# Kernel tuning notes

Hardware: AMD Instinct MI355X
Metric: run time of the kernel (lower is better)

The kernel has to match this reference:

```python
import jax, jax.numpy as jnp
import numpy as np

B, S, D, H = 1, 4096, 512, 8
HD = D // H  # head_dims = 64


def setup_inputs() -> dict:
    key = jax.random.key(0)
    ks = jax.random.split(key, 12)
    scale = 0.02
    query = jax.random.normal(ks[0], (B, S, D), dtype=jnp.float32)
    key_t = jax.random.normal(ks[1], (B, S, D), dtype=jnp.float32)
    value = jax.random.normal(ks[2], (B, S, D), dtype=jnp.float32)
    mask = jax.random.randint(ks[3], (B, 1, S, S), 0, 2, dtype=jnp.int32)
    # per-head projection params (torch Linear: y = x @ W.T + b)
    Wq = jax.random.normal(ks[4], (HD, HD), dtype=jnp.float32) * scale
    bq = jax.random.normal(ks[5], (HD,), dtype=jnp.float32) * scale
    Wk = jax.random.normal(ks[6], (HD, HD), dtype=jnp.float32) * scale
    bk = jax.random.normal(ks[7], (HD,), dtype=jnp.float32) * scale
    Wv = jax.random.normal(ks[8], (HD, HD), dtype=jnp.float32) * scale
    bv = jax.random.normal(ks[9], (HD,), dtype=jnp.float32) * scale
    Wfc = jax.random.normal(ks[10], (D, D), dtype=jnp.float32) * scale
    bfc = jax.random.normal(ks[11], (D,), dtype=jnp.float32) * scale
    return {"query": query, "key": key_t, "value": value, "mask": mask,
            "Wq": Wq, "bq": bq, "Wk": Wk, "bk": bk, "Wv": Wv, "bv": bv,
            "Wfc": Wfc, "bfc": bfc}


def reference(query, key, value, mask, Wq, bq, Wk, bk, Wv, bv, Wfc, bfc):
    Batch, q_len, _ = query.shape
    k_len = key.shape[1]
    # reshape to [b, s, h, d] then apply per-head linear projections
    q = query.reshape(Batch, q_len, H, HD) @ Wq.T + bq
    k = key.reshape(Batch, k_len, H, HD) @ Wk.T + bk
    v = value.reshape(Batch, k_len, H, HD) @ Wv.T + bv
    # raw scores [b, h, q, k]; mask applied BEFORE scaling (as in original)
    score = jnp.einsum('bqhd,bkhd->bhqk', q, k)
    score = jnp.where(mask == 0, jnp.float32(-1e20), score)
    attn = jax.nn.softmax(score / jnp.sqrt(jnp.float32(HD)), axis=-1)
    out = jnp.einsum('bhqv,bvhd->bqhd', attn, v).reshape(Batch, q_len, D)
    return out @ Wfc.T + bfc
```

## Files before the change

### kernel.cpp

```cpp
#include <hip/hip_runtime.h>
#include <hip/hip_bf16.h>

#define S_LEN 4096
#define DMODEL 512
#define NHEAD 8
#define HDIM 64

typedef __bf16 bf16x8 __attribute__((ext_vector_type(8)));
typedef __bf16 bf16x4 __attribute__((ext_vector_type(4)));
typedef float f32x4 __attribute__((ext_vector_type(4)));

#define S2EXP 0.18033688011112042f

__device__ __forceinline__ void gload_lds16(const void* g, void* l) {
    __builtin_amdgcn_global_load_lds((const __attribute__((address_space(1))) void*)g,
                                     (__attribute__((address_space(3))) void*)l, 16, 0, 0);
}

__global__ __launch_bounds__(256) void proj_all_kernel(const float* __restrict__ xq,
                                                       const float* __restrict__ xk,
                                                       const float* __restrict__ xv,
                                                       const float* __restrict__ Wq,
                                                       const float* __restrict__ bq,
                                                       const float* __restrict__ Wk,
                                                       const float* __restrict__ bk,
                                                       const float* __restrict__ Wv,
                                                       const float* __restrict__ bv,
                                                       __bf16* __restrict__ yq,
                                                       __bf16* __restrict__ yk,
                                                       __bf16* __restrict__ vt) {
    __shared__ float T[64][65];
    int bid = blockIdx.x;
    int t = threadIdx.x, wave = t >> 6, lane = t & 63, lg = lane >> 4, lc = lane & 15;
    if (bid < 512) {
        int r0 = bid * 64 + wave * 16;
        const float* xrq = xq + (size_t)(r0 + lc) * 64 + lg * 8;
        const float* xrk = xk + (size_t)(r0 + lc) * 64 + lg * 8;
        bf16x8 aq[2], ak[2];
#pragma unroll
        for (int c = 0; c < 2; ++c) {
            f32x4 u0 = *(const f32x4*)(xrq + c * 32);
            f32x4 u1 = *(const f32x4*)(xrq + c * 32 + 4);
            f32x4 v0 = *(const f32x4*)(xrk + c * 32);
            f32x4 v1 = *(const f32x4*)(xrk + c * 32 + 4);
            bf16x8 a, b;
#pragma unroll
            for (int j = 0; j < 4; ++j) {
                a[j] = (__bf16)u0[j]; a[4 + j] = (__bf16)u1[j];
                b[j] = (__bf16)v0[j]; b[4 + j] = (__bf16)v1[j];
            }
            aq[c] = a; ak[c] = b;
        }
#pragma unroll
        for (int nt = 0; nt < 4; ++nt) {
            const float* wq = Wq + (size_t)(nt * 16 + lc) * 64 + lg * 8;
            const float* wk = Wk + (size_t)(nt * 16 + lc) * 64 + lg * 8;
            f32x4 cq = {0, 0, 0, 0}, ck = {0, 0, 0, 0};
#pragma unroll
            for (int c = 0; c < 2; ++c) {
                f32x4 u0 = *(const f32x4*)(wq + c * 32);
                f32x4 u1 = *(const f32x4*)(wq + c * 32 + 4);
                f32x4 v0 = *(const f32x4*)(wk + c * 32);
                f32x4 v1 = *(const f32x4*)(wk + c * 32 + 4);
                bf16x8 bw, bw2;
#pragma unroll
                for (int j = 0; j < 4; ++j) {
                    bw[j] = (__bf16)u0[j]; bw[4 + j] = (__bf16)u1[j];
                    bw2[j] = (__bf16)v0[j]; bw2[4 + j] = (__bf16)v1[j];
                }
                cq = __builtin_amdgcn_mfma_f32_16x16x32_bf16(aq[c], bw, cq, 0, 0, 0);
                ck = __builtin_amdgcn_mfma_f32_16x16x32_bf16(ak[c], bw2, ck, 0, 0, 0);
            }
            float bqv = bq[nt * 16 + lc], bkv = bk[nt * 16 + lc];
#pragma unroll
            for (int r = 0; r < 4; ++r) {
                yq[(size_t)(r0 + lg * 4 + r) * 64 + nt * 16 + lc] = (__bf16)((cq[r] + bqv) * S2EXP);
                yk[(size_t)(r0 + lg * 4 + r) * 64 + nt * 16 + lc] = (__bf16)(ck[r] + bkv);
            }
        }
    } else {
        int vb = bid - 512;
        int h = vb & 7, s0 = (vb >> 3) * 64;
        const float* xr = xv + ((size_t)(s0 + wave * 16 + lc) * 8 + h) * 64 + lg * 8;
        bf16x8 av[2];
#pragma unroll
        for (int c = 0; c < 2; ++c) {
            f32x4 u0 = *(const f32x4*)(xr + c * 32);
            f32x4 u1 = *(const f32x4*)(xr + c * 32 + 4);
            bf16x8 a;
#pragma unroll
            for (int j = 0; j < 4; ++j) { a[j] = (__bf16)u0[j]; a[4 + j] = (__bf16)u1[j]; }
            av[c] = a;
        }
#pragma unroll
        for (int nt = 0; nt < 4; ++nt) {
            const float* wv = Wv + (size_t)(nt * 16 + lc) * 64 + lg * 8;
            f32x4 cv = {0, 0, 0, 0};
#pragma unroll
            for (int c = 0; c < 2; ++c) {
                f32x4 u0 = *(const f32x4*)(wv + c * 32);
                f32x4 u1 = *(const f32x4*)(wv + c * 32 + 4);
                bf16x8 bw;
#pragma unroll
                for (int j = 0; j < 4; ++j) { bw[j] = (__bf16)u0[j]; bw[4 + j] = (__bf16)u1[j]; }
                cv = __builtin_amdgcn_mfma_f32_16x16x32_bf16(av[c], bw, cv, 0, 0, 0);
            }
            float bvv = bv[nt * 16 + lc];
#pragma unroll
            for (int r = 0; r < 4; ++r) T[wave * 16 + lg * 4 + r][nt * 16 + lc] = cv[r] + bvv;
        }
        __syncthreads();
        int d = t >> 2, qr = t & 3;
        bf16x8 w0, w1;
#pragma unroll
        for (int i = 0; i < 8; ++i) {
            w0[i] = (__bf16)T[qr * 16 + i][d];
            w1[i] = (__bf16)T[qr * 16 + 8 + i][d];
        }
        __bf16* dst = vt + ((size_t)h * 64 + d) * 4096 + s0 + qr * 16;
        *(bf16x8*)(dst) = w0;
        *(bf16x8*)(dst + 8) = w1;
    }
}

__global__ __launch_bounds__(256) void prep_kernel(const int* __restrict__ mask,
                                                   unsigned int* __restrict__ pack,
                                                   const float* __restrict__ Wfc,
                                                   __bf16* __restrict__ wfc_bf) {
    int bid = blockIdx.x;
    int t = threadIdx.x;
    if (bid < 2048) {
        int lane = t & 63;
        int wid = bid * 4 + (t >> 6);
#pragma unroll 4
        for (int it = 0; it < 32; ++it) {
            int gw = wid * 32 + it;
            int qi = gw >> 6, seg = gw & 63;
            unsigned long long bits = __ballot(mask[(size_t)qi * 4096 + seg * 64 + lane] != 0);
            if (lane == 0)
                *(unsigned long long*)(&pack[(size_t)qi * 128 + seg * 2]) = bits;
        }
    } else {
        int b = bid - 2048;
        const f32x4* s4 = (const f32x4*)Wfc;
#pragma unroll
        for (int i = 0; i < 8; ++i) {
            int idx = (b * 8 + i) * 256 + t;
            f32x4 v = s4[idx];
            bf16x4 o;
#pragma unroll
            for (int j = 0; j < 4; ++j) o[j] = (__bf16)v[j];
            *(bf16x4*)(wfc_bf + (size_t)idx * 4) = o;
        }
    }
}

__global__ __launch_bounds__(256, 8) void attn_kernel(const __bf16* __restrict__ qb,
                                                      const __bf16* __restrict__ kb,
                                                      const __bf16* __restrict__ vt,
                                                      const unsigned int* __restrict__ mp,
                                                      int split_steps,
                                                      float* __restrict__ opart,
                                                      float* __restrict__ stats,
                                                      __bf16* __restrict__ ao) {
    int bid = blockIdx.x;
    int h = bid & 7, qt = (bid >> 3) & 63, sp = bid >> 9;
    int kv0 = sp * split_steps * 32;
    int nsteps = min(split_steps, 128 - sp * split_steps);
    int t = threadIdx.x, wave = t >> 6, lane = t & 63, lg = lane >> 4, lc = lane & 15;
    int q0 = qt * 64 + wave * 16;

    __shared__ __bf16 Kt[2][32 * 64];
    __shared__ __bf16 Vt[2][64 * 32];
    __shared__ __bf16 P[4][16 * 32];

    int srK = lane >> 3;
    int cgK = (lane & 7) ^ srK;
    int srV = lane >> 2;
    int cgV = ((lane & 3) - ((lane >> 3) & 3)) & 3;

    const __bf16* qrow = qb + ((size_t)(q0 + lc) * 8 + h) * 64 + lg * 8;
    bf16x8 qf0 = *(const bf16x8*)(qrow);
    bf16x8 qf1 = *(const bf16x8*)(qrow + 32);

    bf16x8 onesf;
#pragma unroll
    for (int j = 0; j < 8; ++j) onesf[j] = (__bf16)1.0f;

    f32x4 o0 = {0,0,0,0}, o1 = {0,0,0,0}, o2 = {0,0,0,0}, o3 = {0,0,0,0};
    f32x4 l_acc = {0,0,0,0};

    const unsigned int* mrow = mp + (size_t)(q0 + lc) * 128;
    const __bf16* vbase = vt + (size_t)h * 64 * 4096;

    gload_lds16(kb + (size_t)(kv0 + wave * 8 + srK) * 512 + h * 64 + cgK * 8, &Kt[0][wave * 512]);
    gload_lds16(vbase + (size_t)(wave * 16 + srV) * 4096 + kv0 + cgV * 8,     &Vt[0][wave * 512]);
    __syncthreads();

    int rotP = (lc >> 1) & 3;
    int lg4 = lg * 4;
    for (int step = 0; step < nsteps; ++step) {
        int cur = step & 1;
        int kb_i = kv0 + step * 32;
        if (step < nsteps - 1) {
            int nxt = kb_i + 32;
            gload_lds16(kb + (size_t)(nxt + wave * 8 + srK) * 512 + h * 64 + cgK * 8, &Kt[cur ^ 1][wave * 512]);
            gload_lds16(vbase + (size_t)(wave * 16 + srV) * 4096 + nxt + cgV * 8,     &Vt[cur ^ 1][wave * 512]);
        }
        const char* Kb = (const char*)&Kt[cur][0];
        f32x4 sc[2];
#pragma unroll
        for (int kc = 0; kc < 2; ++kc) {
            int row = kc * 16 + lc;
            int sw = (row & 7) << 4;
            bf16x8 kf0 = *(const bf16x8*)(Kb + ((row * 128 + lg * 16) ^ sw));
            bf16x8 kf1 = *(const bf16x8*)(Kb + ((row * 128 + 64 + lg * 16) ^ sw));
            f32x4 z = {0,0,0,0};
            z = __builtin_amdgcn_mfma_f32_16x16x32_bf16(kf0, qf0, z, 0, 0, 0);
            z = __builtin_amdgcn_mfma_f32_16x16x32_bf16(kf1, qf1, z, 0, 0, 0);
            sc[kc] = z;
        }
        unsigned int mws = mrow[kb_i >> 5] >> lg4;
        char* pbase = (char*)&P[wave][0];
#pragma unroll
        for (int kc = 0; kc < 2; ++kc) {
            bf16x4 pk;
#pragma unroll
            for (int r = 0; r < 4; ++r) {
                float p = __builtin_amdgcn_exp2f(sc[kc][r]);
                int sel = __builtin_amdgcn_sbfe((int)mws, kc * 16 + r, 1);
                pk[r] = (__bf16)__int_as_float(__float_as_int(p) & sel);
            }
            int phys = ((kc * 2 + (lg >> 1)) + rotP) & 3;
            int byte = lc * 64 + phys * 16 + (lg & 1) * 8;
            *(bf16x4*)(pbase + byte) = pk;
        }
        const char* Vb = (const char*)&Vt[cur][0];
        bf16x8 pf = *(const bf16x8*)(pbase + (lc * 64 + (((lg + rotP) & 3) * 16)));
        l_acc = __builtin_amdgcn_mfma_f32_16x16x32_bf16(pf, onesf, l_acc, 0, 0, 0);
#pragma unroll
        for (int dt = 0; dt < 4; ++dt) {
            int row = dt * 16 + lc;
            bf16x8 vf = *(const bf16x8*)(Vb + (row * 64 + (((lg + rotP) & 3) * 16)));
            if (dt == 0) o0 = __builtin_amdgcn_mfma_f32_16x16x32_bf16(pf, vf, o0, 0, 0, 0);
            if (dt == 1) o1 = __builtin_amdgcn_mfma_f32_16x16x32_bf16(pf, vf, o1, 0, 0, 0);
            if (dt == 2) o2 = __builtin_amdgcn_mfma_f32_16x16x32_bf16(pf, vf, o2, 0, 0, 0);
            if (dt == 3) o3 = __builtin_amdgcn_mfma_f32_16x16x32_bf16(pf, vf, o3, 0, 0, 0);
        }
        __syncthreads();
    }
    if (opart) {
        if (lc == 0) {
#pragma unroll
            for (int r = 0; r < 4; ++r)
                stats[(size_t)sp * 32768 + (size_t)(q0 + lg * 4 + r) * 8 + h] = l_acc[r];
        }
#pragma unroll
        for (int r = 0; r < 4; ++r) {
            size_t rh = (size_t)sp * 32768 + (size_t)(q0 + lg * 4 + r) * 8 + h;
            float* dst = opart + rh * 64;
            dst[0 * 16 + lc] = o0[r];
            dst[1 * 16 + lc] = o1[r];
            dst[2 * 16 + lc] = o2[r];
            dst[3 * 16 + lc] = o3[r];
        }
    } else {
#pragma unroll
        for (int r = 0; r < 4; ++r) {
            float inv = 1.0f / l_acc[r];
            int row = q0 + lg * 4 + r;
            __bf16* dst = ao + (size_t)row * 512 + h * 64;
            dst[0 * 16 + lc] = (__bf16)(o0[r] * inv);
            dst[1 * 16 + lc] = (__bf16)(o1[r] * inv);
            dst[2 * 16 + lc] = (__bf16)(o2[r] * inv);
            dst[3 * 16 + lc] = (__bf16)(o3[r] * inv);
        }
    }
}

__global__ __launch_bounds__(256) void combine_kernel(const float* __restrict__ opart,
                                                      const float* __restrict__ stats,
                                                      __bf16* __restrict__ ao, int nsplit) {
    int t = threadIdx.x, lane = t & 63, w = t >> 6;
    int rh = blockIdx.x * 4 + w;
    float L = 0.f, acc = 0.f;
#pragma unroll 4
    for (int sp = 0; sp < nsplit; ++sp) {
        L += stats[(size_t)sp * 32768 + rh];
        acc += opart[((size_t)sp * 32768 + rh) * 64 + lane];
    }
    int row = rh >> 3, h = rh & 7;
    ao[(size_t)row * 512 + h * 64 + lane] = (__bf16)(acc / L);
}

__global__ __launch_bounds__(256) void fc_kernel(const __bf16* __restrict__ ao,
                                                 const __bf16* __restrict__ Wb,
                                                 const float* __restrict__ bfc,
                                                 float* __restrict__ out) {
    int bid = blockIdx.x;
    int stile = bid >> 3, nt = bid & 7;
    int t = threadIdx.x, wave = t >> 6, lane = t & 63, lg = lane >> 4, lc = lane & 15;
    int s0 = stile * 64 + wave * 16;
    int n0 = nt * 64;
    f32x4 c0 = {0,0,0,0}, c1 = {0,0,0,0}, c2 = {0,0,0,0}, c3 = {0,0,0,0};
    for (int k0 = 0; k0 < 512; k0 += 32) {
        bf16x8 af = *(const bf16x8*)(ao + (size_t)(s0 + lc) * 512 + k0 + lg * 8);
        const __bf16* wb = Wb + k0 + lg * 8;
        c0 = __builtin_amdgcn_mfma_f32_16x16x32_bf16(af, *(const bf16x8*)(wb + (size_t)(n0 + 0 * 16 + lc) * 512), c0, 0, 0, 0);
        c1 = __builtin_amdgcn_mfma_f32_16x16x32_bf16(af, *(const bf16x8*)(wb + (size_t)(n0 + 1 * 16 + lc) * 512), c1, 0, 0, 0);
        c2 = __builtin_amdgcn_mfma_f32_16x16x32_bf16(af, *(const bf16x8*)(wb + (size_t)(n0 + 2 * 16 + lc) * 512), c2, 0, 0, 0);
        c3 = __builtin_amdgcn_mfma_f32_16x16x32_bf16(af, *(const bf16x8*)(wb + (size_t)(n0 + 3 * 16 + lc) * 512), c3, 0, 0, 0);
    }
#pragma unroll
    for (int r = 0; r < 4; ++r) {
        int row = s0 + lg * 4 + r;
        float* dst = out + (size_t)row * 512 + n0;
        dst[0 * 16 + lc] = c0[r] + bfc[n0 + 0 * 16 + lc];
        dst[1 * 16 + lc] = c1[r] + bfc[n0 + 1 * 16 + lc];
        dst[2 * 16 + lc] = c2[r] + bfc[n0 + 2 * 16 + lc];
        dst[3 * 16 + lc] = c3[r] + bfc[n0 + 3 * 16 + lc];
    }
}

extern "C" void kernel_launch(void* const* d_in, const int* in_sizes, int n_in,
                              void* d_out, int out_size, void* d_ws, size_t ws_size,
                              hipStream_t stream) {
    const float* query = (const float*)d_in[0];
    const float* key   = (const float*)d_in[1];
    const float* value = (const float*)d_in[2];
    const int*   mask  = (const int*)d_in[3];
    const float* Wq  = (const float*)d_in[4];
    const float* bq  = (const float*)d_in[5];
    const float* Wk  = (const float*)d_in[6];
    const float* bk  = (const float*)d_in[7];
    const float* Wv  = (const float*)d_in[8];
    const float* bv  = (const float*)d_in[9];
    const float* Wfc = (const float*)d_in[10];
    const float* bfc = (const float*)d_in[11];

    char* ws = (char*)d_ws;
    const size_t MB = 1024 * 1024;
    __bf16* q_bf   = (__bf16*)(ws + 0 * MB);
    __bf16* k_bf   = (__bf16*)(ws + 4 * MB);
    __bf16* vt     = (__bf16*)(ws + 8 * MB);
    __bf16* ao     = (__bf16*)(ws + 12 * MB);
    __bf16* wfc_bf = (__bf16*)(ws + 16 * MB);
    unsigned int* mpack = (unsigned int*)(ws + 17 * MB);
    const size_t base = 19 * MB;
    int nsplit = 1, split_steps = 128;
    if (ws_size >= base + 4 * (8 * MB) + 4 * 131072)      { nsplit = 4; split_steps = 32; }
    else if (ws_size >= base + 2 * (8 * MB) + 2 * 131072) { nsplit = 2; split_steps = 64; }
    float* opart = (float*)(ws + base);
    float* stats = (float*)(ws + base + (size_t)nsplit * 8 * MB);

    proj_all_kernel<<<1024, 256, 0, stream>>>(query, key, value, Wq, bq, Wk, bk, Wv, bv,
                                              q_bf, k_bf, vt);
    prep_kernel<<<2080, 256, 0, stream>>>(mask, mpack, Wfc, wfc_bf);
    if (nsplit > 1) {
        attn_kernel<<<512 * nsplit, 256, 0, stream>>>(q_bf, k_bf, vt, mpack,
                                                      split_steps, opart, stats, ao);
        combine_kernel<<<8192, 256, 0, stream>>>(opart, stats, ao, nsplit);
    } else {
        attn_kernel<<<512, 256, 0, stream>>>(q_bf, k_bf, vt, mpack,
                                             split_steps, nullptr, nullptr, ao);
    }
    fc_kernel<<<512, 256, 0, stream>>>(ao, wfc_bf, bfc, (float*)d_out);
}
```

Measured before the change: 135.1 us.

## Deepen attention KV pipeline to four LDS stages and stage mask via LDS

Replaces the double-buffered K/V staging in the attention kernel with a four-buffer ring that prefetches two steps ahead, using explicit vmcnt waits and a single barrier per step. The loop is unrolled by four. The packed mask words are also loaded into LDS asynchronously instead of read per lane from global memory. Separately, the KV split drops from 4 to 2 and occupancy hint goes from 8 to 4 blocks, which lowers parallelism and combine traffic but increases LDS use per block and the length of each block's serial loop.

Measured after the change: 123.6 us. 8.5% less time.

```diff
diff --git a/kernel.cpp b/kernel.cpp
--- a/kernel.cpp
+++ b/kernel.cpp
@@ -15,6 +15,10 @@
 __device__ __forceinline__ void gload_lds16(const void* g, void* l) {
     __builtin_amdgcn_global_load_lds((const __attribute__((address_space(1))) void*)g,
                                      (__attribute__((address_space(3))) void*)l, 16, 0, 0);
+}
+__device__ __forceinline__ void gload_lds4(const void* g, void* l) {
+    __builtin_amdgcn_global_load_lds((const __attribute__((address_space(1))) void*)g,
+                                     (__attribute__((address_space(3))) void*)l, 4, 0, 0);
 }
 
 __global__ __launch_bounds__(256) void proj_all_kernel(const float* __restrict__ xq,
@@ -155,7 +159,7 @@
     }
 }
 
-__global__ __launch_bounds__(256, 8) void attn_kernel(const __bf16* __restrict__ qb,
+__global__ __launch_bounds__(256, 4) void attn_kernel(const __bf16* __restrict__ qb,
                                                       const __bf16* __restrict__ kb,
                                                       const __bf16* __restrict__ vt,
                                                       const unsigned int* __restrict__ mp,
@@ -166,13 +170,14 @@
     int bid = blockIdx.x;
     int h = bid & 7, qt = (bid >> 3) & 63, sp = bid >> 9;
     int kv0 = sp * split_steps * 32;
-    int nsteps = min(split_steps, 128 - sp * split_steps);
+    int nsteps = split_steps;
     int t = threadIdx.x, wave = t >> 6, lane = t & 63, lg = lane >> 4, lc = lane & 15;
     int q0 = qt * 64 + wave * 16;
 
-    __shared__ __bf16 Kt[2][32 * 64];
-    __shared__ __bf16 Vt[2][64 * 32];
+    __shared__ __bf16 Kt[4][32 * 64];
+    __shared__ __bf16 Vt[4][64 * 32];
     __shared__ __bf16 P[4][16 * 32];
+    __shared__ unsigned int Mld[4][64];
 
     int srK = lane >> 3;
     int cgK = (lane & 7) ^ srK;
@@ -190,65 +195,88 @@
     f32x4 o0 = {0,0,0,0}, o1 = {0,0,0,0}, o2 = {0,0,0,0}, o3 = {0,0,0,0};
     f32x4 l_acc = {0,0,0,0};
 
-    const unsigned int* mrow = mp + (size_t)(q0 + lc) * 128;
     const __bf16* vbase = vt + (size_t)h * 64 * 4096;
-
-    gload_lds16(kb + (size_t)(kv0 + wave * 8 + srK) * 512 + h * 64 + cgK * 8, &Kt[0][wave * 512]);
-    gload_lds16(vbase + (size_t)(wave * 16 + srV) * 4096 + kv0 + cgV * 8,     &Vt[0][wave * 512]);
-    __syncthreads();
+    const unsigned int* mbase = mp + (size_t)(qt * 64 + lane) * 128 + (kv0 >> 5);
 
     int rotP = (lc >> 1) & 3;
     int lg4 = lg * 4;
-    for (int step = 0; step < nsteps; ++step) {
-        int cur = step & 1;
-        int kb_i = kv0 + step * 32;
-        if (step < nsteps - 1) {
-            int nxt = kb_i + 32;
-            gload_lds16(kb + (size_t)(nxt + wave * 8 + srK) * 512 + h * 64 + cgK * 8, &Kt[cur ^ 1][wave * 512]);
-            gload_lds16(vbase + (size_t)(wave * 16 + srV) * 4096 + nxt + cgV * 8,     &Vt[cur ^ 1][wave * 512]);
-        }
-        const char* Kb = (const char*)&Kt[cur][0];
-        f32x4 sc[2];
-#pragma unroll
-        for (int kc = 0; kc < 2; ++kc) {
-            int row = kc * 16 + lc;
-            int sw = (row & 7) << 4;
-            bf16x8 kf0 = *(const bf16x8*)(Kb + ((row * 128 + lg * 16) ^ sw));
-            bf16x8 kf1 = *(const bf16x8*)(Kb + ((row * 128 + 64 + lg * 16) ^ sw));
-            f32x4 z = {0,0,0,0};
-            z = __builtin_amdgcn_mfma_f32_16x16x32_bf16(kf0, qf0, z, 0, 0, 0);
-            z = __builtin_amdgcn_mfma_f32_16x16x32_bf16(kf1, qf1, z, 0, 0, 0);
-            sc[kc] = z;
-        }
-        unsigned int mws = mrow[kb_i >> 5] >> lg4;
-        char* pbase = (char*)&P[wave][0];
-#pragma unroll
-        for (int kc = 0; kc < 2; ++kc) {
-            bf16x4 pk;
-#pragma unroll
-            for (int r = 0; r < 4; ++r) {
-                float p = __builtin_amdgcn_exp2f(sc[kc][r]);
-                int sel = __builtin_amdgcn_sbfe((int)mws, kc * 16 + r, 1);
-                pk[r] = (__bf16)__int_as_float(__float_as_int(p) & sel);
-            }
-            int phys = ((kc * 2 + (lg >> 1)) + rotP) & 3;
-            int byte = lc * 64 + phys * 16 + (lg & 1) * 8;
-            *(bf16x4*)(pbase + byte) = pk;
-        }
-        const char* Vb = (const char*)&Vt[cur][0];
-        bf16x8 pf = *(const bf16x8*)(pbase + (lc * 64 + (((lg + rotP) & 3) * 16)));
-        l_acc = __builtin_amdgcn_mfma_f32_16x16x32_bf16(pf, onesf, l_acc, 0, 0, 0);
-#pragma unroll
-        for (int dt = 0; dt < 4; ++dt) {
-            int row = dt * 16 + lc;
-            bf16x8 vf = *(const bf16x8*)(Vb + (row * 64 + (((lg + rotP) & 3) * 16)));
-            if (dt == 0) o0 = __builtin_amdgcn_mfma_f32_16x16x32_bf16(pf, vf, o0, 0, 0, 0);
-            if (dt == 1) o1 = __builtin_amdgcn_mfma_f32_16x16x32_bf16(pf, vf, o1, 0, 0, 0);
-            if (dt == 2) o2 = __builtin_amdgcn_mfma_f32_16x16x32_bf16(pf, vf, o2, 0, 0, 0);
-            if (dt == 3) o3 = __builtin_amdgcn_mfma_f32_16x16x32_bf16(pf, vf, o3, 0, 0, 0);
-        }
-        __syncthreads();
-    }
+
+#define STAGE(tt, B)                                                                       \
+    {                                                                                      \
+        if (wave == 0) gload_lds4(mbase + (tt), &Mld[B][0]);                               \
+        gload_lds16(kb + (size_t)(kv0 + (tt) * 32 + wave * 8 + srK) * 512 + h * 64 + cgK * 8, \
+                    &Kt[B][wave * 512]);                                                   \
+        gload_lds16(vbase + (size_t)(wave * 16 + srV) * 4096 + kv0 + (tt) * 32 + cgV * 8,  \
+                    &Vt[B][wave * 512]);                                                   \
+    }
+
+    STAGE(0, 0)
+    STAGE(1, 1)
+    asm volatile("s_waitcnt vmcnt(0)" ::: "memory");
+    __builtin_amdgcn_s_barrier();
+
+#define ATTN_STEP(s, C, G)                                                                 \
+    {                                                                                      \
+        if ((s) + 2 < nsteps) STAGE((s) + 2, G)                                            \
+        asm volatile("s_waitcnt vmcnt(4)" ::: "memory");                                   \
+        __builtin_amdgcn_s_barrier();                                                      \
+        unsigned int mws = Mld[C][wave * 16 + lc] >> lg4;                                  \
+        const char* Kb = (const char*)&Kt[C][0];                                           \
+        f32x4 sc0 = {0,0,0,0}, sc1 = {0,0,0,0};                                            \
+        {                                                                                  \
+            int row = lc, sw = (row & 7) << 4;                                             \
+            bf16x8 kf0 = *(const bf16x8*)(Kb + ((row * 128 + lg * 16) ^ sw));              \
+            bf16x8 kf1 = *(const bf16x8*)(Kb + ((row * 128 + 64 + lg * 16) ^ sw));         \
+            sc0 = __builtin_amdgcn_mfma_f32_16x16x32_bf16(kf0, qf0, sc0, 0, 0, 0);         \
+            sc0 = __builtin_amdgcn_mfma_f32_16x16x32_bf16(kf1, qf1, sc0, 0, 0, 0);         \
+        }                                                                                  \
+        {                                                                                  \
+            int row = 16 + lc, sw = (row & 7) << 4;                                        \
+            bf16x8 kf0 = *(const bf16x8*)(Kb + ((row * 128 + lg * 16) ^ sw));              \
+            bf16x8 kf1 = *(const bf16x8*)(Kb + ((row * 128 + 64 + lg * 16) ^ sw));         \
+            sc1 = __builtin_amdgcn_mfma_f32_16x16x32_bf16(kf0, qf0, sc1, 0, 0, 0);         \
+            sc1 = __builtin_amdgcn_mfma_f32_16x16x32_bf16(kf1, qf1, sc1, 0, 0, 0);         \
+        }                                                                                  \
+        char* pbase = (char*)&P[wave][0];                                                  \
+        {                                                                                  \
+            bf16x4 pk0, pk1;                                                               \
+            _Pragma("unroll")                                                              \
+            for (int r = 0; r < 4; ++r) {                                                  \
+                float pa = __builtin_amdgcn_exp2f(sc0[r]);                                 \
+                int sa = __builtin_amdgcn_sbfe((int)mws, r, 1);                            \
+                pk0[r] = (__bf16)__int_as_float(__float_as_int(pa) & sa);                  \
+                float pb = __builtin_amdgcn_exp2f(sc1[r]);                                 \
+                int sb = __builtin_amdgcn_sbfe((int)mws, 16 + r, 1);                       \
+                pk1[r] = (__bf16)__int_as_float(__float_as_int(pb) & sb);                  \
+            }                                                                              \
+            int ph0 = (((lg >> 1)) + rotP) & 3;                                            \
+            int ph1 = ((2 + (lg >> 1)) + rotP) & 3;                                        \
+            *(bf16x4*)(pbase + lc * 64 + ph0 * 16 + (lg & 1) * 8) = pk0;                   \
+            *(bf16x4*)(pbase + lc * 64 + ph1 * 16 + (lg & 1) * 8) = pk1;                   \
+        }                                                                                  \
+        const char* Vb = (const char*)&Vt[C][0];                                           \
+        bf16x8 pf = *(const bf16x8*)(pbase + (lc * 64 + (((lg + rotP) & 3) * 16)));        \
+        l_acc = __builtin_amdgcn_mfma_f32_16x16x32_bf16(pf, onesf, l_acc, 0, 0, 0);        \
+        _Pragma("unroll")                                                                  \
+        for (int dt = 0; dt < 4; ++dt) {                                                   \
+            int row = dt * 16 + lc;                                                        \
+            bf16x8 vf = *(const bf16x8*)(Vb + (row * 64 + (((lg + rotP) & 3) * 16)));      \
+            if (dt == 0) o0 = __builtin_amdgcn_mfma_f32_16x16x32_bf16(pf, vf, o0, 0, 0, 0);\
+            if (dt == 1) o1 = __builtin_amdgcn_mfma_f32_16x16x32_bf16(pf, vf, o1, 0, 0, 0);\
+            if (dt == 2) o2 = __builtin_amdgcn_mfma_f32_16x16x32_bf16(pf, vf, o2, 0, 0, 0);\
+            if (dt == 3) o3 = __builtin_amdgcn_mfma_f32_16x16x32_bf16(pf, vf, o3, 0, 0, 0);\
+        }                                                                                  \
+    }
+
+    for (int s = 0; s < nsteps; s += 4) {
+        ATTN_STEP(s + 0, 0, 2)
+        ATTN_STEP(s + 1, 1, 3)
+        ATTN_STEP(s + 2, 2, 0)
+        ATTN_STEP(s + 3, 3, 1)
+    }
+#undef ATTN_STEP
+#undef STAGE
+
     if (opart) {
         if (lc == 0) {
 #pragma unroll
@@ -284,7 +312,7 @@
     int t = threadIdx.x, lane = t & 63, w = t >> 6;
     int rh = blockIdx.x * 4 + w;
     float L = 0.f, acc = 0.f;
-#pragma unroll 4
+#pragma unroll 2
     for (int sp = 0; sp < nsplit; ++sp) {
         L += stats[(size_t)sp * 32768 + rh];
         acc += opart[((size_t)sp * 32768 + rh) * 64 + lane];
@@ -347,9 +375,7 @@
     __bf16* wfc_bf = (__bf16*)(ws + 16 * MB);
     unsigned int* mpack = (unsigned int*)(ws + 17 * MB);
     const size_t base = 19 * MB;
-    int nsplit = 1, split_steps = 128;
-    if (ws_size >= base + 4 * (8 * MB) + 4 * 131072)      { nsplit = 4; split_steps = 32; }
-    else if (ws_size >= base + 2 * (8 * MB) + 2 * 131072) { nsplit = 2; split_steps = 64; }
+    int nsplit = (ws_size >= base + 2 * (8 * MB) + 2 * 131072) ? 2 : 1;
     float* opart = (float*)(ws + base);
     float* stats = (float*)(ws + base + (size_t)nsplit * 8 * MB);
 
@@ -358,11 +384,11 @@
     prep_kernel<<<2080, 256, 0, stream>>>(mask, mpack, Wfc, wfc_bf);
     if (nsplit > 1) {
         attn_kernel<<<512 * nsplit, 256, 0, stream>>>(q_bf, k_bf, vt, mpack,
-                                                      split_steps, opart, stats, ao);
+                                                      S_LEN / nsplit / 32, opart, stats, ao);
         combine_kernel<<<8192, 256, 0, stream>>>(opart, stats, ao, nsplit);
     } else {
         attn_kernel<<<512, 256, 0, stream>>>(q_bf, k_bf, vt, mpack,
-                                             split_steps, nullptr, nullptr, ao);
+                                             128, nullptr, nullptr, ao);
     }
     fc_kernel<<<512, 256, 0, stream>>>(ao, wfc_bf, bfc, (float*)d_out);
 }
```
